# Kernel tuning notes

Measured on AMD Instinct MI355X. Metric: run time of the kernel, lower is better.

Reference implementation:

```python
import jax, jax.numpy as jnp
import numpy as np

B, S, H, W, E, NH = 8, 16, 32, 32, 128, 8
HD = E // NH
EPS = 1e-5


def setup_inputs() -> dict:
    key = jax.random.key(0)
    ks = jax.random.split(key, 6)
    sc = lambda fan: 1.0 / np.sqrt(fan).astype(np.float32)
    return {
        "inputs": jax.random.normal(ks[0], (B, S, H, W, E), jnp.float32),
        "W_proj": jax.random.normal(ks[1], (E, E), jnp.float32) * sc(E),
        "ln_gamma": jnp.ones((E,), jnp.float32),
        "ln_beta": jnp.zeros((E,), jnp.float32),
        "W_in": jax.random.normal(ks[2], (E, 3 * E), jnp.float32) * sc(E),
        "W_out": jax.random.normal(ks[3], (E, E), jnp.float32) * sc(E),
        "conv_k": jax.random.normal(ks[4], (4 * E, 2 * E, 3, 3), jnp.float32) * sc(2 * E * 9),
    }


def reference(inputs, W_proj, ln_gamma, ln_beta, W_in, W_out, conv_k):
    # x = silu(project(inputs))
    x = jax.nn.silu(inputs @ W_proj)
    # LayerNorm over last dim
    mu = x.mean(-1, keepdims=True)
    var = x.var(-1, keepdims=True)
    x = (x - mu) * jax.lax.rsqrt(var + EPS) * ln_gamma + ln_beta
    # Multi-head attention over the sequence dim, batched over (b, h, w)
    qkv = (x @ W_in).reshape(B, S, H, W, NH, 3 * HD)
    q, k, v = jnp.split(qkv, 3, axis=-1)
    scale = 1.0 / np.sqrt(HD).astype(np.float32)
    scores = jnp.einsum('bshwid,blhwid->bhwisl', q, k) * scale  # (B,H,W,NH,S,S)
    tril = jnp.tril(jnp.ones((S, S), jnp.float32))
    # faithful to source: +1.0 on/below diagonal, -1000.0 above
    mask = tril * 1.0 + (1.0 - tril) * (-1000.0)
    attnw = jax.nn.softmax(scores + mask, axis=-1)
    ao = jnp.einsum('bhwisl,blhwid->bshwid', attnw, v).reshape(B, S, H, W, E)
    x = ao @ W_out + inputs  # residual
    # ConvLSTM over seq: (B,S,H,W,E) -> (S,B,E,H,W) for scan
    xc = jnp.transpose(x, (1, 0, 4, 2, 3))
    h0 = jnp.zeros((B, E, H, W), x.dtype)
    c0 = jnp.zeros((B, E, H, W), x.dtype)

    def step(carry, xt):
        h, c = carry
        comb = jnp.concatenate([xt, h], axis=1)  # (B, 2E, H, W)
        cc = jax.lax.conv_general_dilated(
            comb, conv_k, window_strides=(1, 1), padding='SAME',
            dimension_numbers=('NCHW', 'OIHW', 'NCHW'))
        ci, cf, co, cg = jnp.split(cc, 4, axis=1)
        c_next = jax.nn.sigmoid(cf) * c + jax.nn.sigmoid(ci) * jnp.tanh(cg)
        h_next = jax.nn.sigmoid(co) * jnp.tanh(c_next)
        return (h_next, c_next), h_next

    _, outs = jax.lax.scan(step, (h0, c0), xc)  # (S,B,E,H,W)
    return jnp.transpose(outs, (1, 0, 3, 4, 2))  # (B,S,H,W,E)
```

## Files before the change

### kernel.cpp

```cpp
#include <hip/hip_runtime.h>
#include <math.h>

#define B_  8
#define S_  16
#define H_  32
#define W_  32
#define E_  128
#define NH_ 8
#define HD_ 16
#define HW_ (H_*W_)
#define NTOK (B_*S_*H_*W_)

typedef __attribute__((ext_vector_type(8))) short short8;
typedef __attribute__((ext_vector_type(4))) short short4v;
typedef __attribute__((ext_vector_type(4))) float floatx4;

__device__ __forceinline__ float sigf(float x){
    return 1.f/(1.f+__expf(-x));
}
__device__ __forceinline__ float tanh_fast(float x){
    x = fminf(fmaxf(x, -15.f), 15.f);
    float e = __expf(2.f*x);
    return (e-1.f)/(e+1.f);
}
__device__ __forceinline__ unsigned short f2bf(float f){
    unsigned int u = __float_as_uint(f);
    u = (u + 0x7fffu + ((u >> 16) & 1u)) >> 16;
    return (unsigned short)u;
}
__device__ __forceinline__ float bf2f(unsigned short h){
    return __uint_as_float(((unsigned int)h) << 16);
}

__device__ __forceinline__ void st_gate(float* p, float v){ *p = v; }
__device__ __forceinline__ void st_gate(unsigned short* p, float v){ *p = f2bf(v); }
__device__ __forceinline__ void load_gate(const float* p, float* o){
    float4 v = *(const float4*)p; o[0]=v.x; o[1]=v.y; o[2]=v.z; o[3]=v.w;
}
__device__ __forceinline__ void load_gate(const unsigned short* p, float* o){
    ushort4 v = *(const ushort4*)p;
    o[0]=bf2f(v.x); o[1]=bf2f(v.y); o[2]=bf2f(v.z); o[3]=bf2f(v.w);
}

__global__ __launch_bounds__(256)
void k_pack_wproj(const float* __restrict__ Wp, short* __restrict__ Wpp){
    int p = blockIdx.x*256 + threadIdx.x;
    int L = p & 63;
    int idx = p >> 6;
    int nt = idx / 12, kb = idx - nt*12;
    int n = nt*16 + (L & 15);
    int kr = (kb & 3)*32 + (L >> 4)*8;
    bool lo = (kb >= 8);
    short8 v;
    #pragma unroll
    for (int j=0;j<8;j++){
        float wv = Wp[(kr+j)*128 + n];
        unsigned short h = f2bf(wv);
        v[j] = lo ? (short)f2bf(wv - bf2f(h)) : (short)h;
    }
    *(short8*)&Wpp[(long)p*8] = v;
}

__global__ __launch_bounds__(256,2)
void k_proj_ln_mfma(const float* __restrict__ in, const short* __restrict__ Wpp,
                    const float* __restrict__ gamma, const float* __restrict__ beta,
                    float* __restrict__ X){
    __shared__ short As[64*264];
    int tid = threadIdx.x;
    int w = tid >> 6, L = tid & 63;
    int quad = L >> 4, lm = L & 15;
    long r0 = (long)blockIdx.x * 64;

    {
        int c = (tid & 31)*4;
        int rbase = tid >> 5;
        #pragma unroll
        for (int rr=0; rr<8; rr++){
            int r = rr*8 + rbase;
            float4 v = *(const float4*)&in[(r0 + r)*128 + c];
            short4v hv, lv;
            unsigned short h;
            h = f2bf(v.x); hv[0]=(short)h; lv[0]=(short)f2bf(v.x - bf2f(h));
            h = f2bf(v.y); hv[1]=(short)h; lv[1]=(short)f2bf(v.y - bf2f(h));
            h = f2bf(v.z); hv[2]=(short)h; lv[2]=(short)f2bf(v.z - bf2f(h));
            h = f2bf(v.w); hv[3]=(short)h; lv[3]=(short)f2bf(v.w - bf2f(h));
            *(short4v*)&As[r*264 + c] = hv;
            *(short4v*)&As[r*264 + 128 + c] = lv;
        }
    }
    __syncthreads();

    floatx4 acc[8];
    #pragma unroll
    for (int nt=0;nt<8;nt++) acc[nt] = (floatx4){0.f,0.f,0.f,0.f};
    const short8* Bp8 = (const short8*)Wpp;
    int arow = (w*16 + lm)*264 + quad*8;
    #pragma unroll
    for (int kb=0; kb<12; kb++){
        int off = (kb<4) ? kb*32 : ((kb<8) ? 128+(kb-4)*32 : (kb-8)*32);
        short8 af = *(const short8*)&As[arow + off];
        #pragma unroll
        for (int nt=0;nt<8;nt++){
            short8 bf = Bp8[(nt*12+kb)*64 + L];
            acc[nt] = __builtin_amdgcn_mfma_f32_16x16x32_bf16(af, bf, acc[nt], 0,0,0);
        }
    }

    float g[8], bb[8];
    #pragma unroll
    for (int nt=0;nt<8;nt++){ g[nt]=gamma[nt*16+lm]; bb[nt]=beta[nt*16+lm]; }
    float s1[4]={0,0,0,0}, s2[4]={0,0,0,0};
    #pragma unroll
    for (int nt=0;nt<8;nt++)
        #pragma unroll
        for (int r=0;r<4;r++){
            float a = acc[nt][r];
            float si = a*sigf(a);
            acc[nt][r] = si;
            s1[r] += si; s2[r] += si*si;
        }
    #pragma unroll
    for (int d=1; d<16; d<<=1)
        #pragma unroll
        for (int r=0;r<4;r++){
            s1[r] += __shfl_xor(s1[r], d);
            s2[r] += __shfl_xor(s2[r], d);
        }
    float mu[4], rs[4];
    #pragma unroll
    for (int r=0;r<4;r++){
        mu[r] = s1[r]*(1.f/128.f);
        float var = s2[r]*(1.f/128.f) - mu[r]*mu[r];
        rs[r] = rsqrtf(var + 1e-5f);
    }
    #pragma unroll
    for (int nt=0;nt<8;nt++)
        #pragma unroll
        for (int r=0;r<4;r++){
            long row = r0 + w*16 + quad*4 + r;
            X[row*128 + nt*16 + lm] = (acc[nt][r]-mu[r])*rs[r]*g[nt] + bb[nt];
        }
}

__global__ __launch_bounds__(256)
void k_pack_win(const float* __restrict__ Win, short* __restrict__ Winp){
    int p = blockIdx.x*256 + threadIdx.x;
    int L = p & 63;
    int idx = p >> 6;
    int nt = idx >> 2, kc = idx & 3;
    int n = nt*16 + (L & 15);
    int k0 = kc*32 + (L >> 4)*8;
    short8 v;
    #pragma unroll
    for (int j=0;j<8;j++) v[j] = (short)f2bf(Win[(k0+j)*384 + n]);
    *(short8*)&Winp[(long)p*8] = v;
}

__global__ __launch_bounds__(256)
void k_pack_wout(const float* __restrict__ Wout, short* __restrict__ Woutp){
    int p = blockIdx.x*256 + threadIdx.x;
    int L = p & 63;
    int idx = p >> 6;
    int h = idx >> 3, nt = idx & 7;
    int n = nt*16 + (L & 15);
    int k0 = (L >> 4)*8;
    short8 v;
    #pragma unroll
    for (int j=0;j<8;j++){
        int k = k0 + j;
        v[j] = (k < 16) ? (short)f2bf(Wout[(h*16+k)*128 + n]) : (short)0;
    }
    *(short8*)&Woutp[(long)p*8] = v;
}

__global__ __launch_bounds__(256,5)
void k_attn_mfma(const float* __restrict__ X, const short* __restrict__ Winp,
                 const short* __restrict__ Woutp, const float* __restrict__ resid,
                 float* __restrict__ Y){
    __shared__ short lds[16000];
    const int XO=0;
    const int QO=8704;
    const int KO=10240;
    const int VO=11776;
    const int PO=12928;
    const int AOO=14464;
    int tid = threadIdx.x;
    int w = tid >> 6, L = tid & 63;
    int quad = L >> 4, lm = L & 15;
    int b = blockIdx.x >> 8, tile = blockIdx.x & 255;
    int hw0 = tile * 4;
    int hw = hw0 + w;

    {
        int cq = L & 31, rh = L >> 5;
        for (int p=0; p<8; p++){
            int m = w*16 + p*2 + rh;
            int s = m & 15;
            float4 v = *(const float4*)&X[((((long)b*16 + s)*1024) + hw)*128 + cq*4];
            short4v hv;
            hv[0]=(short)f2bf(v.x); hv[1]=(short)f2bf(v.y);
            hv[2]=(short)f2bf(v.z); hv[3]=(short)f2bf(v.w);
            *(short4v*)&lds[XO + m*136 + cq*4] = hv;
        }
    }

    floatx4 Oa[8];
    #pragma unroll
    for (int nt=0;nt<8;nt++) Oa[nt] = (floatx4){0.f,0.f,0.f,0.f};

    const floatx4 zc = (floatx4){0.f,0.f,0.f,0.f};
    const short8 z8 = {0,0,0,0,0,0,0,0};
    int m0 = w*16;

    for (int h=0; h<8; h++){
        floatx4 qacc[3];
        #pragma unroll
        for (int t=0;t<3;t++) qacc[t] = zc;
        #pragma unroll
        for (int kc=0;kc<4;kc++){
            short8 af = *(const short8*)&lds[XO + (m0+lm)*136 + kc*32 + quad*8];
            #pragma unroll
            for (int t=0;t<3;t++){
                int nt = 3*h + t;
                short8 bf = *(const short8*)&Winp[(long)((nt*4+kc)*64 + L)*8];
                qacc[t] = __builtin_amdgcn_mfma_f32_16x16x32_bf16(af, bf, qacc[t], 0,0,0);
            }
        }
        #pragma unroll
        for (int r=0;r<4;r++){
            lds[QO + (m0+quad*4+r)*24 + lm] = (short)f2bf(qacc[0][r]);
            lds[KO + (m0+quad*4+r)*24 + lm] = (short)f2bf(qacc[1][r]);
        }
        {
            short4v vv;
            #pragma unroll
            for (int r=0;r<4;r++) vv[r] = (short)f2bf(qacc[2][r]);
            *(short4v*)&lds[VO + lm*72 + m0 + quad*4] = vv;
        }

        {
            short8 qf = z8, kf = z8;
            if (quad < 2){
                qf = *(const short8*)&lds[QO + (m0+lm)*24 + quad*8];
                kf = *(const short8*)&lds[KO + (m0+lm)*24 + quad*8];
            }
            floatx4 scv = __builtin_amdgcn_mfma_f32_16x16x32_bf16(qf, kf, zc, 0,0,0);
            float pv[4], mr[4];
            #pragma unroll
            for (int r=0;r<4;r++){
                int si = quad*4 + r;
                pv[r] = scv[r]*0.25f + (lm <= si ? 1.0f : -1000.0f);
                mr[r] = pv[r];
            }
            #pragma unroll
            for (int d=1; d<16; d<<=1)
                #pragma unroll
                for (int r=0;r<4;r++) mr[r] = fmaxf(mr[r], __shfl_xor(mr[r], d));
            float ex[4], sm[4];
            #pragma unroll
            for (int r=0;r<4;r++){ ex[r] = __expf(pv[r]-mr[r]); sm[r] = ex[r]; }
            #pragma unroll
            for (int d=1; d<16; d<<=1)
                #pragma unroll
                for (int r=0;r<4;r++) sm[r] += __shfl_xor(sm[r], d);
            #pragma unroll
            for (int r=0;r<4;r++)
                lds[PO + (m0+quad*4+r)*24 + lm] = (short)f2bf(ex[r]/sm[r]);

            short8 pf = z8, vf = z8;
            if (quad < 2){
                pf = *(const short8*)&lds[PO + (m0+lm)*24 + quad*8];
                vf = *(const short8*)&lds[VO + lm*72 + m0 + quad*8];
            }
            floatx4 aov = __builtin_amdgcn_mfma_f32_16x16x32_bf16(pf, vf, zc, 0,0,0);
            #pragma unroll
            for (int r=0;r<4;r++)
                lds[AOO + (m0+quad*4+r)*24 + lm] = (short)f2bf(aov[r]);
        }

        {
            short8 aof = z8;
            if (quad < 2)
                aof = *(const short8*)&lds[AOO + (m0+lm)*24 + quad*8];
            #pragma unroll
            for (int nt=0;nt<8;nt++){
                short8 wf = *(const short8*)&Woutp[(long)((h*8+nt)*64 + L)*8];
                Oa[nt] = __builtin_amdgcn_mfma_f32_16x16x32_bf16(aof, wf, Oa[nt], 0,0,0);
            }
        }
    }

    #pragma unroll
    for (int nt=0;nt<8;nt++){
        int n = nt*16 + lm;
        #pragma unroll
        for (int r=0;r<4;r++){
            int s = quad*4 + r;
            long addr = (((long)b*16 + s)*1024 + hw)*128 + n;
            Y[addr] = Oa[nt][r] + resid[addr];
        }
    }
}

__global__ __launch_bounds__(256)
void k_pack_w(const float* __restrict__ ck, short* __restrict__ Bp){
    int p = blockIdx.x*256 + threadIdx.x;
    int L = p & 63;
    int nt = (p >> 6) & 31;
    int c32 = (p >> 11) & 7;
    int tap = p >> 14;
    int oc = nt*16 + (L & 15);
    int kq = L >> 4;
    short8 v;
    #pragma unroll
    for (int j=0;j<8;j++){
        int ic = c32*32 + kq*8 + j;
        v[j] = (short)f2bf(ck[(oc*256+ic)*9 + tap]);
    }
    *(short8*)&Bp[(long)p*8] = v;
}

__global__ __launch_bounds__(256)
void k_pack_x(const float* __restrict__ X, short* __restrict__ xh, int s, int zero_h){
    int idx = blockIdx.x*256 + threadIdx.x;
    int row = idx >> 4;
    int ch = (idx & 15) * 8;
    int b = row >> 10, hw = row & 1023;
    const float* src = X + (((long)(b*16+s)*1024 + hw)*128 + ch);
    float4 a = *(const float4*)src;
    float4 c = *(const float4*)(src+4);
    short8 v;
    v[0]=(short)f2bf(a.x); v[1]=(short)f2bf(a.y); v[2]=(short)f2bf(a.z); v[3]=(short)f2bf(a.w);
    v[4]=(short)f2bf(c.x); v[5]=(short)f2bf(c.y); v[6]=(short)f2bf(c.z); v[7]=(short)f2bf(c.w);
    *(short8*)&xh[(long)row*256 + ch] = v;
    if (zero_h){
        short8 z = {0,0,0,0,0,0,0,0};
        *(short8*)&xh[(long)row*256 + 128 + ch] = z;
    }
}

template<typename GT>
__global__ __launch_bounds__(256,2)
void k_conv_mfma(const short* __restrict__ xh, const short* __restrict__ Bp,
                 GT* __restrict__ gbuf){
    __shared__ short As[4*34*264];
    int tid = threadIdx.x;
    int Nblk = blockIdx.x & 3, g = blockIdx.x >> 2;
    int b = g >> 4, y0 = (g & 15)*2;
    int w = tid >> 6, L = tid & 63;
    int quad = L >> 4, lm = L & 15;
    int ntg = Nblk*8 + w*2;

    const short8 z8 = {0,0,0,0,0,0,0,0};
    for (int i=0; i<17; i++){
        int pidx = i*256 + tid;
        int cb  = pidx & 31;
        int pos = pidx >> 5;
        int row = pos / 34;
        int xp  = pos - row*34;
        int yy = y0 - 1 + row, xx = xp - 1;
        short8 v = z8;
        if (yy>=0 && yy<32 && xx>=0 && xx<32)
            v = *(const short8*)&xh[(((long)(b*32+yy)*32+xx)<<8) + cb*8];
        *(short8*)&As[(row*34+xp)*264 + cb*8] = v;
    }
    __syncthreads();

    floatx4 acc[4][2];
    #pragma unroll
    for (int mt=0;mt<4;mt++)
        #pragma unroll
        for (int nti=0;nti<2;nti++)
            acc[mt][nti] = (floatx4){0.f,0.f,0.f,0.f};

    const short8* Bp8 = (const short8*)Bp;

    for (int tap=0; tap<9; tap++){
        int dy = tap/3 - 1, dx = tap - (tap/3)*3 - 1;
        int abase[4];
        #pragma unroll
        for (int mt=0;mt<4;mt++){
            int ys = mt >> 1;
            int x  = (mt & 1)*16 + lm;
            abase[mt] = (((ys+dy+1)*34) + x + dx + 1)*264 + quad*8;
        }
        #pragma unroll
        for (int sic=0; sic<4; sic++){
            #pragma unroll
            for (int c2=0; c2<2; c2++){
                short8 bfr[2];
                #pragma unroll
                for (int nti=0;nti<2;nti++)
                    bfr[nti] = Bp8[((tap*8 + sic*2 + c2)*32 + ntg + nti)*64 + L];
                #pragma unroll
                for (int mt=0;mt<4;mt++){
                    short8 afr = *(const short8*)&As[abase[mt] + sic*64 + c2*32];
                    #pragma unroll
                    for (int nti=0;nti<2;nti++)
                        acc[mt][nti] = __builtin_amdgcn_mfma_f32_16x16x32_bf16(afr, bfr[nti], acc[mt][nti], 0,0,0);
                }
            }
        }
    }

    #pragma unroll
    for (int mt=0;mt<4;mt++){
        #pragma unroll
        for (int nti=0;nti<2;nti++){
            int n = Nblk*128 + (w*2+nti)*16 + lm;
            #pragma unroll
            for (int r=0;r<4;r++){
                long row = (long)g*64 + mt*16 + quad*4 + r;
                st_gate(&gbuf[row*512 + n], acc[mt][nti][r]);
            }
        }
    }
}

template<typename GT>
__global__ __launch_bounds__(256)
void k_lstm(const GT* __restrict__ gbuf, float* __restrict__ cbuf,
            float* __restrict__ X, short* __restrict__ xh, int s){
    int idx = blockIdx.x*256 + threadIdx.x;
    int row = idx >> 5;
    int c4 = (idx & 31)*4;
    float gi[4], gf[4], go[4], gg[4];
    const GT* gp = gbuf + (long)row*512 + c4;
    load_gate(gp,       gi);
    load_gate(gp + 128, gf);
    load_gate(gp + 256, go);
    load_gate(gp + 384, gg);
    float co[4];
    if (s == 0){ co[0]=co[1]=co[2]=co[3]=0.f; }
    else {
        float4 cv = *(const float4*)&cbuf[(long)row*128 + c4];
        co[0]=cv.x; co[1]=cv.y; co[2]=cv.z; co[3]=cv.w;
    }
    float cn[4], hn[4];
    #pragma unroll
    for (int j=0;j<4;j++){
        cn[j] = sigf(gf[j])*co[j] + sigf(gi[j])*tanh_fast(gg[j]);
        hn[j] = sigf(go[j])*tanh_fast(cn[j]);
    }
    *(float4*)&cbuf[(long)row*128 + c4] = make_float4(cn[0],cn[1],cn[2],cn[3]);
    int b = row >> 10, hw = row & 1023;
    long xoff = (((long)(b*16+s)*1024 + hw)*128) + c4;
    *(float4*)&X[xoff] = make_float4(hn[0],hn[1],hn[2],hn[3]);
    ushort4 hv;
    hv.x = f2bf(hn[0]); hv.y = f2bf(hn[1]); hv.z = f2bf(hn[2]); hv.w = f2bf(hn[3]);
    *(ushort4*)&xh[(long)row*256 + 128 + c4] = hv;
    if (s < 15){
        long x2 = (((long)(b*16+s+1)*1024 + hw)*128) + c4;
        float4 xv = *(const float4*)&X[x2];
        ushort4 xb;
        xb.x = f2bf(xv.x); xb.y = f2bf(xv.y); xb.z = f2bf(xv.z); xb.w = f2bf(xv.w);
        *(ushort4*)&xh[(long)row*256 + c4] = xb;
    }
}

extern "C" void kernel_launch(void* const* d_in, const int* in_sizes, int n_in,
                              void* d_out, int out_size, void* d_ws, size_t ws_size,
                              hipStream_t stream){
    const float* inputs = (const float*)d_in[0];
    const float* Wp     = (const float*)d_in[1];
    const float* gamma  = (const float*)d_in[2];
    const float* beta   = (const float*)d_in[3];
    const float* Win    = (const float*)d_in[4];
    const float* Wout   = (const float*)d_in[5];
    const float* ck     = (const float*)d_in[6];
    float* X = (float*)d_out;

    char* ws = (char*)d_ws;
    const size_t szB    = 147456ull*16;
    const size_t szXH   = 8192ull*256*2;
    const size_t szC    = 8192ull*128*4;
    const size_t szWin  = 6144ull*16;
    const size_t szWout = 4096ull*16;
    short* Bp    = (short*)(ws);
    short* xh    = (short*)(ws + szB);
    float* cbuf  = (float*)(ws + szB + szXH);
    short* Winp  = (short*)(ws + szB + szXH + szC);
    short* Woutp = (short*)(ws + szB + szXH + szC + szWin);
    char*  gch   =         ws + szB + szXH + szC + szWin + szWout;
    bool gate_f32 = ws_size >= (szB + szXH + szC + szWin + szWout + 8192ull*512*4);
    short* Wprojp = (short*)gch;

    k_pack_w<<<576, 256, 0, stream>>>(ck, Bp);
    k_pack_win<<<24, 256, 0, stream>>>(Win, Winp);
    k_pack_wout<<<16, 256, 0, stream>>>(Wout, Woutp);
    k_pack_wproj<<<24, 256, 0, stream>>>(Wp, Wprojp);
    k_proj_ln_mfma<<<NTOK/64, 256, 0, stream>>>(inputs, Wprojp, gamma, beta, X);
    k_attn_mfma<<<2048, 256, 0, stream>>>(X, Winp, Woutp, inputs, X);
    k_pack_x<<<512, 256, 0, stream>>>(X, xh, 0, 1);

    if (gate_f32){
        float* gbuf = (float*)gch;
        for (int s=0; s<16; s++){
            k_conv_mfma<float><<<512, 256, 0, stream>>>(xh, Bp, gbuf);
            k_lstm<float><<<1024, 256, 0, stream>>>(gbuf, cbuf, X, xh, s);
        }
    } else {
        unsigned short* gbuf = (unsigned short*)gch;
        for (int s=0; s<16; s++){
            k_conv_mfma<unsigned short><<<512, 256, 0, stream>>>(xh, Bp, gbuf);
            k_lstm<unsigned short><<<1024, 256, 0, stream>>>(gbuf, cbuf, X, xh, s);
        }
    }
}
```

Baseline: 924.6 us.

## Widen conv blocks to 512 threads covering 256 output channels

```diff
diff --git a/kernel.cpp b/kernel.cpp
--- a/kernel.cpp
+++ b/kernel.cpp
@@ -340,78 +340,93 @@
 }
 
 template<typename GT>
-__global__ __launch_bounds__(256,2)
+__global__ __launch_bounds__(512,2)
 void k_conv_mfma(const short* __restrict__ xh, const short* __restrict__ Bp,
                  GT* __restrict__ gbuf){
     __shared__ short As[4*34*264];
     int tid = threadIdx.x;
-    int Nblk = blockIdx.x & 3, g = blockIdx.x >> 2;
+    int Nblk = blockIdx.x & 1, g = blockIdx.x >> 1;
     int b = g >> 4, y0 = (g & 15)*2;
     int w = tid >> 6, L = tid & 63;
     int quad = L >> 4, lm = L & 15;
-    int ntg = Nblk*8 + w*2;
+    int wm = w >> 2, wn = w & 3;
+    int ntg = Nblk*16 + wn*4;
 
     const short8 z8 = {0,0,0,0,0,0,0,0};
-    for (int i=0; i<17; i++){
-        int pidx = i*256 + tid;
-        int cb  = pidx & 31;
-        int pos = pidx >> 5;
-        int row = pos / 34;
-        int xp  = pos - row*34;
-        int yy = y0 - 1 + row, xx = xp - 1;
-        short8 v = z8;
-        if (yy>=0 && yy<32 && xx>=0 && xx<32)
-            v = *(const short8*)&xh[(((long)(b*32+yy)*32+xx)<<8) + cb*8];
-        *(short8*)&As[(row*34+xp)*264 + cb*8] = v;
+    {
+        short8 vs[9];
+        #pragma unroll
+        for (int i=0; i<9; i++){
+            int pidx = i*512 + tid;
+            short8 v = z8;
+            if (pidx < 4352){
+                int cb  = pidx & 31;
+                int pos = pidx >> 5;
+                int row = pos / 34;
+                int xp  = pos - row*34;
+                int yy = y0 - 1 + row, xx = xp - 1;
+                if (yy>=0 && yy<32 && xx>=0 && xx<32)
+                    v = *(const short8*)&xh[(((long)(b*32+yy)*32+xx)<<8) + cb*8];
+            }
+            vs[i] = v;
+        }
+        #pragma unroll
+        for (int i=0; i<9; i++){
+            int pidx = i*512 + tid;
+            if (pidx < 4352){
+                int cb  = pidx & 31;
+                int pos = pidx >> 5;
+                *(short8*)&As[pos*264 + cb*8] = vs[i];
+            }
+        }
     }
     __syncthreads();
 
-    floatx4 acc[4][2];
-    #pragma unroll
-    for (int mt=0;mt<4;mt++)
-        #pragma unroll
-        for (int nti=0;nti<2;nti++)
-            acc[mt][nti] = (floatx4){0.f,0.f,0.f,0.f};
+    floatx4 acc[2][4];
+    #pragma unroll
+    for (int mtl=0;mtl<2;mtl++)
+        #pragma unroll
+        for (int nti=0;nti<4;nti++)
+            acc[mtl][nti] = (floatx4){0.f,0.f,0.f,0.f};
 
     const short8* Bp8 = (const short8*)Bp;
 
     for (int tap=0; tap<9; tap++){
         int dy = tap/3 - 1, dx = tap - (tap/3)*3 - 1;
-        int abase[4];
-        #pragma unroll
-        for (int mt=0;mt<4;mt++){
-            int ys = mt >> 1;
-            int x  = (mt & 1)*16 + lm;
-            abase[mt] = (((ys+dy+1)*34) + x + dx + 1)*264 + quad*8;
+        int abase[2];
+        #pragma unroll
+        for (int mtl=0;mtl<2;mtl++){
+            int x = mtl*16 + lm;
+            abase[mtl] = (((wm+dy+1)*34) + x + dx + 1)*264 + quad*8;
         }
         #pragma unroll
         for (int sic=0; sic<4; sic++){
             #pragma unroll
             for (int c2=0; c2<2; c2++){
-                short8 bfr[2];
+                short8 bfr[4];
                 #pragma unroll
-                for (int nti=0;nti<2;nti++)
+                for (int nti=0;nti<4;nti++)
                     bfr[nti] = Bp8[((tap*8 + sic*2 + c2)*32 + ntg + nti)*64 + L];
                 #pragma unroll
-                for (int mt=0;mt<4;mt++){
-                    short8 afr = *(const short8*)&As[abase[mt] + sic*64 + c2*32];
+                for (int mtl=0;mtl<2;mtl++){
+                    short8 afr = *(const short8*)&As[abase[mtl] + sic*64 + c2*32];
                     #pragma unroll
-                    for (int nti=0;nti<2;nti++)
-                        acc[mt][nti] = __builtin_amdgcn_mfma_f32_16x16x32_bf16(afr, bfr[nti], acc[mt][nti], 0,0,0);
+                    for (int nti=0;nti<4;nti++)
+                        acc[mtl][nti] = __builtin_amdgcn_mfma_f32_16x16x32_bf16(afr, bfr[nti], acc[mtl][nti], 0,0,0);
                 }
             }
         }
     }
 
     #pragma unroll
-    for (int mt=0;mt<4;mt++){
-        #pragma unroll
-        for (int nti=0;nti<2;nti++){
-            int n = Nblk*128 + (w*2+nti)*16 + lm;
+    for (int mtl=0;mtl<2;mtl++){
+        #pragma unroll
+        for (int nti=0;nti<4;nti++){
+            int n = Nblk*256 + (wn*4+nti)*16 + lm;
             #pragma unroll
             for (int r=0;r<4;r++){
-                long row = (long)g*64 + mt*16 + quad*4 + r;
-                st_gate(&gbuf[row*512 + n], acc[mt][nti][r]);
+                long row = (long)g*64 + (wm*2+mtl)*16 + quad*4 + r;
+                st_gate(&gbuf[row*512 + n], acc[mtl][nti][r]);
             }
         }
     }
@@ -496,13 +511,13 @@
     if (gate_f32){
         float* gbuf = (float*)gch;
         for (int s=0; s<16; s++){
-            k_conv_mfma<float><<<512, 256, 0, stream>>>(xh, Bp, gbuf);
+            k_conv_mfma<float><<<256, 512, 0, stream>>>(xh, Bp, gbuf);
             k_lstm<float><<<1024, 256, 0, stream>>>(gbuf, cbuf, X, xh, s);
         }
     } else {
         unsigned short* gbuf = (unsigned short*)gch;
         for (int s=0; s<16; s++){
-            k_conv_mfma<unsigned short><<<512, 256, 0, stream>>>(xh, Bp, gbuf);
+            k_conv_mfma<unsigned short><<<256, 512, 0, stream>>>(xh, Bp, gbuf);
             k_lstm<unsigned short><<<1024, 256, 0, stream>>>(gbuf, cbuf, X, xh, s);
         }
     }
```

Result: faster. 871.4 us (-5.8%).
